# Kernel optimization log

Hardware: AMD Instinct MI355X
Metric: run time of the kernel (lower is better)

## Reference

```python
import jax, jax.numpy as jnp
import numpy as np

B, S, H, E, R, K = 8, 2048, 2048, 8, 16, 3
ALPHA = 0.5
LAMBDA_COV = 0.5
BETA_ENT = 0.1
TEMP_LO, TEMP_HI = 0.5, 1.5
SCALE_T = 2.0   # lora scaling (alpha/r) teacher
SCALE_S = 2.0   # lora scaling student
EPS = 1e-8


def setup_inputs() -> dict:
    key = jax.random.key(0)
    ks = jax.random.split(key, 16)
    tg = jax.random.uniform(ks[0], (B, S, E)) + 1e-3
    tg = tg / tg.sum(-1, keepdims=True)            # teacher gate probabilities
    sg = jax.random.uniform(ks[1], (B, S, E)) + 1e-3
    sg = sg / sg.sum(-1, keepdims=True)            # student gate probabilities
    th = jax.random.normal(ks[2], (B, S, H), jnp.float32)
    sh = jax.random.normal(ks[3], (B, S, H), jnp.float32)
    mask = jnp.ones((B, S), jnp.int32)
    un = jax.random.uniform(ks[4], (K, B, S, E))   # MC sampling noise
    inv = 1.0 / np.sqrt(H)
    W_t = jax.random.normal(ks[5], (H, H), jnp.float32) * inv
    b_t = jnp.zeros((H,), jnp.float32)
    A_t = jax.random.normal(ks[6], (R, H), jnp.float32) * 0.02
    B_t = jax.random.normal(ks[7], (E, H, R), jnp.float32) * 0.02
    W_s = jax.random.normal(ks[8], (H, H), jnp.float32) * inv
    b_s = jnp.zeros((H,), jnp.float32)
    A_s = jax.random.normal(ks[9], (R, H), jnp.float32) * 0.02
    B_s = jax.random.normal(ks[10], (E, H, R), jnp.float32) * 0.02
    temperature = jnp.float32(1.0)
    return dict(teacher_gates=tg, student_gates=sg,
                teacher_hidden_states=th, student_hidden_states=sh,
                attention_mask=mask, uniform_noise=un,
                W_t=W_t, b_t=b_t, A_t=A_t, B_t=B_t,
                W_s=W_s, b_s=b_s, A_s=A_s, B_s=B_s,
                temperature=temperature)


def _mse_all_experts(th, sh, W_t, b_t, A_t, B_t, W_s, b_s, A_s, B_s):
    """MSE(student_expert_hidden, teacher_expert_hidden) for ALL experts at once.
    expert_hidden = x@W^T + b + scale * (x@A^T) @ B_e^T. Expanding the squared
    difference avoids materializing [B,S,E,H]."""
    base_t = th @ W_t.T + b_t                      # [B,S,H]
    base_s = sh @ W_s.T + b_s                      # [B,S,H]
    a_t = th @ A_t.T                               # [B,S,R]
    a_s = sh @ A_s.T                               # [B,S,R]
    d = base_s - base_t                            # [B,S,H]
    mean_base = jnp.mean(d * d, axis=-1)           # [B,S]
    # cross terms: (1/H) d . (scale * a @ B_e^T)
    proj_s = jnp.einsum('bsh,ehr->bser', d, B_s)   # [B,S,E,R]
    proj_t = jnp.einsum('bsh,ehr->bser', d, B_t)
    cross = SCALE_S * jnp.einsum('bser,bsr->bse', proj_s, a_s) \
          - SCALE_T * jnp.einsum('bser,bsr->bse', proj_t, a_t)
    # quadratic lora terms via per-expert Gram matrices [E,R,R]
    G_ss = jnp.einsum('ehr,ehq->erq', B_s, B_s)
    G_st = jnp.einsum('ehr,ehq->erq', B_s, B_t)
    G_tt = jnp.einsum('ehr,ehq->erq', B_t, B_t)
    q_ss = jnp.einsum('bsr,erq,bsq->bse', a_s, G_ss, a_s)
    q_st = jnp.einsum('bsr,erq,bsq->bse', a_s, G_st, a_t)
    q_tt = jnp.einsum('bsr,erq,bsq->bse', a_t, G_tt, a_t)
    quad = SCALE_S * SCALE_S * q_ss - 2.0 * SCALE_S * SCALE_T * q_st + SCALE_T * SCALE_T * q_tt
    return mean_base[..., None] + (2.0 / H) * cross + (1.0 / H) * quad  # [B,S,E]


def _method_a(teacher_gates, student_gates, mse_all, uniform_noise, mask_f):
    """Vectorized MC expert sampling with alpha-renormalization (lax.scan over K)."""
    gumbel = -jnp.log(-jnp.log(uniform_noise * (1.0 - 2e-7) + 1e-7))  # [K,B,S,E]

    def step(p, g):  # p: current (renormalized) probs [B,S,E]
        idx = jnp.argmax(jnp.log(p) + g, axis=-1)          # multinomial sample [B,S]
        oh = jax.nn.one_hot(idx, E, dtype=p.dtype)          # [B,S,E]
        w = jnp.sum(p * oh, -1)                             # importance weight [B,S]
        mse_k = jnp.sum(mse_all * oh, -1)                   # gathered expert MSE
        sg_k = jnp.sum(student_gates * oh, -1)              # student gate at sampled expert
        mw = mask_f * w
        feat = jnp.sum(mw * mse_k)
        wsum = jnp.sum(mw)
        t_counts = jnp.sum(mw[..., None] * oh, axis=(0, 1))           # [E]
        s_counts = jnp.sum((mask_f * sg_k)[..., None] * oh, axis=(0, 1))
        p_new = p * (1.0 + (ALPHA - 1.0) * oh)
        p_new = p_new / jnp.sum(p_new, -1, keepdims=True)
        return p_new, (feat, wsum, t_counts, s_counts)

    _, (feats, wsums, tcs, scs) = jax.lax.scan(step, teacher_gates, gumbel)
    total_feat = feats.sum()
    total_w = wsums.sum()
    t_counts = tcs.sum(0)
    s_counts = scs.sum(0)

    feat_loss = total_feat / jnp.maximum(total_w, 1e-8)
    t_avg = t_counts / t_counts.sum() + EPS
    s_avg = s_counts / s_counts.sum() + EPS
    t_avg = t_avg / t_avg.sum()
    s_avg = s_avg / s_avg.sum()
    # F.kl_div(s.log(), t, reduction='batchmean') on 1-D input divides by E
    coverage_kl = jnp.sum(t_avg * (jnp.log(t_avg) - jnp.log(s_avg))) / E
    return feat_loss, coverage_kl


def reference(teacher_gates, student_gates, teacher_hidden_states, student_hidden_states,
              attention_mask, uniform_noise, W_t, b_t, A_t, B_t, W_s, b_s, A_s, B_s,
              temperature):
    mask_f = attention_mask.astype(teacher_gates.dtype)
    mse_all = _mse_all_experts(teacher_hidden_states, student_hidden_states,
                               W_t, b_t, A_t, B_t, W_s, b_s, A_s, B_s)
    feat_loss, coverage_kl = _method_a(teacher_gates, student_gates, mse_all,
                                       uniform_noise, mask_f)
    method_a_total = feat_loss + LAMBDA_COV * coverage_kl
    # Method B: temperature-entropy router distillation
    temp_c = jnp.clip(temperature, TEMP_LO, TEMP_HI)
    s_temp = jax.nn.softmax(student_gates / temp_c, axis=-1)
    # F.kl_div(s_temp.log(), teacher, 'batchmean') divides by batch dim B
    temp_kl = jnp.sum(teacher_gates * (jnp.log(teacher_gates) - jnp.log(s_temp))) / B
    entropy = -jnp.sum(student_gates * jnp.log(student_gates), axis=-1)
    entropy_loss = -jnp.mean(entropy)
    method_b_total = temp_kl + BETA_ENT * entropy_loss
    # [feat, coverage_kl, method_a_total, temp_kl, entropy, method_b_total, temperature]
    return jnp.stack([feat_loss, coverage_kl, method_a_total,
                      temp_kl, entropy_loss, method_b_total, temp_c])
```

## Files before the change

kernel.cpp:

```cpp
#include <hip/hip_runtime.h>
#include <math.h>

typedef unsigned short u16;
typedef unsigned int u32;
typedef float f32x4 __attribute__((ext_vector_type(4)));
typedef __bf16 bf16x8 __attribute__((ext_vector_type(8)));

#define NTOK 16384
#define HD   2048
#define KX   4096
#define NW   2176
#define NB   256

__device__ __forceinline__ u16 f2bf(float f) {
  u32 u = __float_as_uint(f);
  u32 r = (u + 0x7fffu + ((u >> 16) & 1u)) >> 16;
  return (u16)r;
}
__device__ __forceinline__ float bf2f(u16 s) { return __uint_as_float(((u32)s) << 16); }

__device__ __forceinline__ void gload_lds16(const void* g, void* l) {
  __builtin_amdgcn_global_load_lds((const __attribute__((address_space(1))) u32*)g,
                                   (__attribute__((address_space(3))) u32*)l, 16, 0, 0);
}

__global__ void zero_accum_k(float* a) {
  if (threadIdx.x < 32) a[threadIdx.x] = 0.f;
}

__global__ void make_bias_k(const float* __restrict__ b_t, const float* __restrict__ b_s,
                            float* __restrict__ db) {
  int i = blockIdx.x * 256 + threadIdx.x;
  if (i < HD) db[i] = b_s[i] - b_t[i];
}

__global__ __launch_bounds__(256) void convert_X_k(const float* __restrict__ th,
                                                   const float* __restrict__ sh,
                                                   u16* __restrict__ X) {
  size_t t = (size_t)blockIdx.x * 256 + threadIdx.x;
  int n = (int)(t >> 9);
  int k = ((int)t & 511) * 8;
  const float* src = (k < HD) ? (th + (size_t)n * HD + k) : (sh + (size_t)n * HD + (k - HD));
  float4 v0 = *(const float4*)src;
  float4 v1 = *(const float4*)(src + 4);
  uint4 pk;
  pk.x = (u32)f2bf(v0.x) | ((u32)f2bf(v0.y) << 16);
  pk.y = (u32)f2bf(v0.z) | ((u32)f2bf(v0.w) << 16);
  pk.z = (u32)f2bf(v1.x) | ((u32)f2bf(v1.y) << 16);
  pk.w = (u32)f2bf(v1.z) | ((u32)f2bf(v1.w) << 16);
  *(uint4*)(X + t * 8) = pk;
}

__global__ __launch_bounds__(256) void convert_W_k(const float* __restrict__ W_t,
                                                   const float* __restrict__ W_s,
                                                   const float* __restrict__ A_t,
                                                   const float* __restrict__ A_s,
                                                   u16* __restrict__ Wc) {
  size_t t = (size_t)blockIdx.x * 256 + threadIdx.x;
  int nr = (int)(t >> 9);
  int k = ((int)t & 511) * 8;
  float f[8];
#pragma unroll
  for (int j = 0; j < 8; ++j) f[j] = 0.f;
  if (nr < HD) {
    if (k < HD) {
      const float* s = W_t + (size_t)nr * HD + k;
#pragma unroll
      for (int j = 0; j < 8; ++j) f[j] = -s[j];
    } else {
      const float* s = W_s + (size_t)nr * HD + (k - HD);
#pragma unroll
      for (int j = 0; j < 8; ++j) f[j] = s[j];
    }
  } else if (nr < HD + 16) {
    if (k < HD) {
      const float* s = A_t + (size_t)(nr - HD) * HD + k;
#pragma unroll
      for (int j = 0; j < 8; ++j) f[j] = s[j];
    }
  } else if (nr < HD + 32) {
    if (k >= HD) {
      const float* s = A_s + (size_t)(nr - HD - 16) * HD + (k - HD);
#pragma unroll
      for (int j = 0; j < 8; ++j) f[j] = s[j];
    }
  }
  uint4 pk;
  pk.x = (u32)f2bf(f[0]) | ((u32)f2bf(f[1]) << 16);
  pk.y = (u32)f2bf(f[2]) | ((u32)f2bf(f[3]) << 16);
  pk.z = (u32)f2bf(f[4]) | ((u32)f2bf(f[5]) << 16);
  pk.w = (u32)f2bf(f[6]) | ((u32)f2bf(f[7]) << 16);
  *(uint4*)(Wc + t * 8) = pk;
}

__global__ __launch_bounds__(256) void convert_Bc_k(const float* __restrict__ Bs_,
                                                    const float* __restrict__ Bt_,
                                                    u16* __restrict__ Bc) {
  size_t t = (size_t)blockIdx.x * 256 + threadIdx.x;
  int c = (int)(t >> 8);
  int h = ((int)t & 255) * 8;
  const float* src = (c < 128) ? Bs_ : Bt_;
  int e = (c & 127) >> 4, r = c & 15;
  const float* base = src + (size_t)e * HD * 16 + (size_t)h * 16 + r;
  float f[8];
#pragma unroll
  for (int j = 0; j < 8; ++j) f[j] = base[(size_t)j * 16];
  uint4 pk;
  pk.x = (u32)f2bf(f[0]) | ((u32)f2bf(f[1]) << 16);
  pk.y = (u32)f2bf(f[2]) | ((u32)f2bf(f[3]) << 16);
  pk.z = (u32)f2bf(f[4]) | ((u32)f2bf(f[5]) << 16);
  pk.w = (u32)f2bf(f[6]) | ((u32)f2bf(f[7]) << 16);
  *(uint4*)(Bc + t * 8) = pk;
}

__global__ __launch_bounds__(256) void gram_k(const float* __restrict__ Bs_,
                                              const float* __restrict__ Bt_,
                                              float* __restrict__ grams) {
  __shared__ float ss[128 * 16];
  __shared__ float st[128 * 16];
  const int e = blockIdx.x;
  const int tid = threadIdx.x;
  const float* bs = Bs_ + (size_t)e * HD * 16;
  const float* bt = Bt_ + (size_t)e * HD * 16;
  const int r = tid >> 4, q = tid & 15;
  float gss = 0.f, gst = 0.f, gtt = 0.f;
  for (int h0 = 0; h0 < HD; h0 += 128) {
    __syncthreads();
#pragma unroll
    for (int j = 0; j < 8; ++j) {
      int i = tid + j * 256;
      ss[i] = bs[(size_t)h0 * 16 + i];
      st[i] = bt[(size_t)h0 * 16 + i];
    }
    __syncthreads();
    for (int hh = 0; hh < 128; ++hh) {
      float vsr = ss[hh * 16 + r], vsq = ss[hh * 16 + q];
      float vtr = st[hh * 16 + r], vtq = st[hh * 16 + q];
      gss += vsr * vsq;
      gst += vsr * vtq;
      gtt += vtr * vtq;
    }
  }
  grams[e * 256 + r * 16 + q] = gss;
  grams[2048 + e * 256 + r * 16 + q] = gst;
  grams[4096 + e * 256 + r * 16 + q] = gtt;
}

template <bool OUT_BF16>
__global__ __launch_bounds__(256) void gemm_bt_k(const u16* __restrict__ A, int lda,
                                                 const u16* __restrict__ Bm, int ldb,
                                                 int K, void* __restrict__ Cp, int ldc,
                                                 const float* __restrict__ bias, int bias_n) {
  __shared__ u16 As[128 * 32];
  __shared__ u16 Bs[128 * 32];
  const int tid = threadIdx.x;
  const int wave = tid >> 6;
  const int lane = tid & 63;
  const int m0 = blockIdx.x * 128;
  const int n0 = blockIdx.y * 128;
  const int wm = (wave >> 1) * 64;
  const int wn = (wave & 1) * 64;
  f32x4 acc[4][4] = {};

  const int srow = wave * 32 + (lane >> 2);
  const int scol = (lane & 3) * 8;
  const u16* gA = A + (size_t)(m0 + srow) * lda + scol;
  const u16* gB = Bm + (size_t)(n0 + srow) * ldb + scol;
  u16* lA = As + wave * 1024;
  u16* lB = Bs + wave * 1024;

  for (int k0 = 0; k0 < K; k0 += 32) {
    gload_lds16(gA + k0, lA);
    gload_lds16(gA + k0 + (size_t)16 * lda, lA + 512);
    gload_lds16(gB + k0, lB);
    gload_lds16(gB + k0 + (size_t)16 * ldb, lB + 512);
    __syncthreads();
    bf16x8 af[4], bff[4];
#pragma unroll
    for (int mi = 0; mi < 4; ++mi)
      af[mi] = *(const bf16x8*)&As[(wm + mi * 16 + (lane & 15)) * 32 + (lane >> 4) * 8];
#pragma unroll
    for (int ni = 0; ni < 4; ++ni)
      bff[ni] = *(const bf16x8*)&Bs[(wn + ni * 16 + (lane & 15)) * 32 + (lane >> 4) * 8];
#pragma unroll
    for (int mi = 0; mi < 4; ++mi)
#pragma unroll
      for (int ni = 0; ni < 4; ++ni)
        acc[mi][ni] = __builtin_amdgcn_mfma_f32_16x16x32_bf16(af[mi], bff[ni], acc[mi][ni], 0, 0, 0);
    __syncthreads();
  }

#pragma unroll
  for (int mi = 0; mi < 4; ++mi) {
#pragma unroll
    for (int ni = 0; ni < 4; ++ni) {
      int row0 = m0 + wm + mi * 16 + (lane >> 4) * 4;
      int col = n0 + wn + ni * 16 + (lane & 15);
      float badd = 0.f;
      if (bias != nullptr && col < bias_n) badd = bias[col];
      f32x4 v = acc[mi][ni];
#pragma unroll
      for (int j = 0; j < 4; ++j) {
        float x = v[j] + badd;
        if (OUT_BF16)
          ((u16*)Cp)[(size_t)(row0 + j) * ldc + col] = f2bf(x);
        else
          ((float*)Cp)[(size_t)(row0 + j) * ldc + col] = x;
      }
    }
  }
}

__global__ __launch_bounds__(256) void token_k(const u16* __restrict__ D,
                                               const float* __restrict__ proj,
                                               const float* __restrict__ grams,
                                               const float* __restrict__ tg,
                                               const float* __restrict__ sg,
                                               const float* __restrict__ un,
                                               const int* __restrict__ maskp,
                                               const float* __restrict__ temp,
                                               float* __restrict__ accum) {
  __shared__ float blk[20];
  if (threadIdx.x < 20) blk[threadIdx.x] = 0.f;
  __syncthreads();
  const int wave = threadIdx.x >> 6, lane = threadIdx.x & 63;
  const int n = blockIdx.x * 4 + wave;
  const u16* drow = D + (size_t)n * NW;

  float ssum = 0.f;
#pragma unroll
  for (int j = 0; j < 4; ++j) {
    uint4 v = *(const uint4*)(drow + j * 512 + lane * 8);
    u32 w;
    float f;
    w = v.x; f = bf2f((u16)(w & 0xffff)); ssum += f * f; f = bf2f((u16)(w >> 16)); ssum += f * f;
    w = v.y; f = bf2f((u16)(w & 0xffff)); ssum += f * f; f = bf2f((u16)(w >> 16)); ssum += f * f;
    w = v.z; f = bf2f((u16)(w & 0xffff)); ssum += f * f; f = bf2f((u16)(w >> 16)); ssum += f * f;
    w = v.w; f = bf2f((u16)(w & 0xffff)); ssum += f * f; f = bf2f((u16)(w >> 16)); ssum += f * f;
  }
#pragma unroll
  for (int m = 1; m < 64; m <<= 1) ssum += __shfl_xor(ssum, m);
  const float mean_base = ssum * (1.0f / (float)HD);

  float a_tv[16], a_sv[16];
#pragma unroll
  for (int r = 0; r < 16; ++r) {
    a_tv[r] = bf2f(drow[HD + r]);
    a_sv[r] = bf2f(drow[HD + 16 + r]);
  }

  const int e = lane & 7;
  const int pp = lane >> 3;
  const float* Ps = proj + (size_t)n * 256 + e * 16;
  const float* Pt = Ps + 128;
  const float* Gss = grams + e * 256;
  const float* Gst = grams + 2048 + e * 256;
  const float* Gtt = grams + 4096 + e * 256;
  float crossp = 0.f, qss = 0.f, qst = 0.f, qtt = 0.f;
#pragma unroll
  for (int rr = 0; rr < 2; ++rr) {
    int r = pp * 2 + rr;
    float asr = bf2f(drow[HD + 16 + r]);
    float atr = bf2f(drow[HD + r]);
    crossp += 2.0f * Ps[r] * asr - 2.0f * Pt[r] * atr;
    const float* gssr = Gss + r * 16;
    const float* gstr = Gst + r * 16;
    const float* gttr = Gtt + r * 16;
    float vss = 0.f, vst = 0.f, vtt = 0.f;
#pragma unroll
    for (int q = 0; q < 16; ++q) {
      vss += gssr[q] * a_sv[q];
      vst += gstr[q] * a_tv[q];
      vtt += gttr[q] * a_tv[q];
    }
    qss += asr * vss;
    qst += asr * vst;
    qtt += atr * vtt;
  }
#pragma unroll
  for (int m = 8; m < 64; m <<= 1) {
    crossp += __shfl_xor(crossp, m);
    qss += __shfl_xor(qss, m);
    qst += __shfl_xor(qst, m);
    qtt += __shfl_xor(qtt, m);
  }
  float quad = 4.0f * qss - 8.0f * qst + 4.0f * qtt;
  float my_mse = mean_base + (2.0f / (float)HD) * crossp + (1.0f / (float)HD) * quad;

  float p[8], gt[8], gs[8];
#pragma unroll
  for (int i = 0; i < 8; ++i) {
    gt[i] = tg[(size_t)n * 8 + i];
    gs[i] = sg[(size_t)n * 8 + i];
    p[i] = gt[i];
  }
  const float mf = (float)maskp[n];
  float feat = 0.f, wsum = 0.f;
  float tc[8] = {0, 0, 0, 0, 0, 0, 0, 0};
  float sc[8] = {0, 0, 0, 0, 0, 0, 0, 0};
#pragma unroll
  for (int k = 0; k < 3; ++k) {
    int idx = 0;
    float best = -1e30f;
#pragma unroll
    for (int i = 0; i < 8; ++i) {
      float u = un[((size_t)k * NTOK + n) * 8 + i];
      float g = -logf(-logf(u * (1.0f - 2e-7f) + 1e-7f));
      float s = logf(p[i]) + g;
      if (s > best) { best = s; idx = i; }
    }
    float w = 0.f, sgi = 0.f;
#pragma unroll
    for (int i = 0; i < 8; ++i)
      if (i == idx) { w = p[i]; sgi = gs[i]; }
    float mse_k = __shfl(my_mse, idx);
    feat += mf * w * mse_k;
    wsum += mf * w;
#pragma unroll
    for (int i = 0; i < 8; ++i)
      if (i == idx) { tc[i] += mf * w; sc[i] += mf * sgi; }
    float sum = 0.f;
#pragma unroll
    for (int i = 0; i < 8; ++i) {
      if (i == idx) p[i] *= 0.5f;
      sum += p[i];
    }
#pragma unroll
    for (int i = 0; i < 8; ++i) p[i] /= sum;
  }

  float tcl = fminf(fmaxf(temp[0], 0.5f), 1.5f);
  float invt = 1.0f / tcl;
  float x[8];
  float xm = -1e30f;
#pragma unroll
  for (int i = 0; i < 8; ++i) { x[i] = gs[i] * invt; xm = fmaxf(xm, x[i]); }
  float sx = 0.f;
#pragma unroll
  for (int i = 0; i < 8; ++i) sx += expf(x[i] - xm);
  float lse = xm + logf(sx);
  float tkl = 0.f, ent = 0.f;
#pragma unroll
  for (int i = 0; i < 8; ++i) {
    tkl += gt[i] * (logf(gt[i]) - (x[i] - lse));
    ent -= gs[i] * logf(gs[i]);
  }

  if (lane == 0) {
    atomicAdd(&blk[0], feat);
    atomicAdd(&blk[1], wsum);
#pragma unroll
    for (int i = 0; i < 8; ++i) {
      atomicAdd(&blk[2 + i], tc[i]);
      atomicAdd(&blk[10 + i], sc[i]);
    }
    atomicAdd(&blk[18], tkl);
    atomicAdd(&blk[19], ent);
  }
  __syncthreads();
  if (threadIdx.x < 20) atomicAdd(&accum[threadIdx.x], blk[threadIdx.x]);
}

__global__ void finalize_k(const float* __restrict__ accum, const float* __restrict__ temp,
                           float* __restrict__ out) {
  if (threadIdx.x != 0 || blockIdx.x != 0) return;
  float feat = accum[0] / fmaxf(accum[1], 1e-8f);
  float tsum = 0.f, ssum = 0.f;
  for (int e2 = 0; e2 < 8; ++e2) { tsum += accum[2 + e2]; ssum += accum[10 + e2]; }
  float ta[8], sa[8];
  float tas = 0.f, sas = 0.f;
  for (int e2 = 0; e2 < 8; ++e2) {
    ta[e2] = accum[2 + e2] / tsum + 1e-8f; tas += ta[e2];
    sa[e2] = accum[10 + e2] / ssum + 1e-8f; sas += sa[e2];
  }
  float cov = 0.f;
  for (int e2 = 0; e2 < 8; ++e2) {
    float tt = ta[e2] / tas, sv = sa[e2] / sas;
    cov += tt * (logf(tt) - logf(sv));
  }
  cov /= 8.0f;
  float tcl = fminf(fmaxf(temp[0], 0.5f), 1.5f);
  float tkl = accum[18] / 8.0f;
  float entl = -accum[19] / (float)NTOK;
  out[0] = feat;
  out[1] = cov;
  out[2] = feat + 0.5f * cov;
  out[3] = tkl;
  out[4] = entl;
  out[5] = tkl + 0.1f * entl;
  out[6] = tcl;
}

extern "C" void kernel_launch(void* const* d_in, const int* in_sizes, int n_in,
                              void* d_out, int out_size, void* d_ws, size_t ws_size,
                              hipStream_t stream) {
  const float* tg = (const float*)d_in[0];
  const float* sg = (const float*)d_in[1];
  const float* th = (const float*)d_in[2];
  const float* sh = (const float*)d_in[3];
  const int* mask = (const int*)d_in[4];
  const float* un = (const float*)d_in[5];
  const float* W_t = (const float*)d_in[6];
  const float* b_t = (const float*)d_in[7];
  const float* A_t = (const float*)d_in[8];
  const float* B_t = (const float*)d_in[9];
  const float* W_s = (const float*)d_in[10];
  const float* b_s = (const float*)d_in[11];
  const float* A_s = (const float*)d_in[12];
  const float* B_s = (const float*)d_in[13];
  const float* temp = (const float*)d_in[14];
  float* out = (float*)d_out;

  char* ws = (char*)d_ws;
  const size_t OFF_X = 0;
  const size_t OFF_W = OFF_X + (size_t)NTOK * KX * 2;
  const size_t OFF_D = OFF_W + (size_t)NW * KX * 2;
  const size_t OFF_BC = OFF_D + (size_t)NTOK * NW * 2;
  const size_t OFF_PJ = OFF_BC + (size_t)NB * HD * 2;
  const size_t OFF_GR = OFF_PJ + (size_t)NTOK * 256 * 4;
  const size_t OFF_AC = OFF_GR + 6144 * 4;
  const size_t OFF_BI = OFF_AC + 128;

  u16* X = (u16*)(ws + OFF_X);
  u16* Wc = (u16*)(ws + OFF_W);
  u16* D = (u16*)(ws + OFF_D);
  u16* Bc = (u16*)(ws + OFF_BC);
  float* proj = (float*)(ws + OFF_PJ);
  float* grams = (float*)(ws + OFF_GR);
  float* accum = (float*)(ws + OFF_AC);
  float* dbias = (float*)(ws + OFF_BI);

  zero_accum_k<<<1, 64, 0, stream>>>(accum);
  make_bias_k<<<8, 256, 0, stream>>>(b_t, b_s, dbias);
  convert_X_k<<<32768, 256, 0, stream>>>(th, sh, X);
  convert_W_k<<<4352, 256, 0, stream>>>(W_t, W_s, A_t, A_s, Wc);
  convert_Bc_k<<<256, 256, 0, stream>>>(B_s, B_t, Bc);
  gram_k<<<8, 256, 0, stream>>>(B_s, B_t, grams);

  gemm_bt_k<true><<<dim3(128, 17), 256, 0, stream>>>(X, KX, Wc, KX, KX, (void*)D, NW, dbias, HD);
  gemm_bt_k<false><<<dim3(128, 2), 256, 0, stream>>>(D, NW, Bc, HD, HD, (void*)proj, 256, nullptr, 0);

  token_k<<<4096, 256, 0, stream>>>(D, proj, grams, tg, sg, un, mask, temp, accum);
  finalize_k<<<1, 64, 0, stream>>>(accum, temp, out);
}
```

Before: 915.0 us.

## Add 256x256 double-buffered swizzled GEMM and split LoRA-A projection out

The main 16384x2176x4096 GEMM is replaced by a dedicated 256x256-tile kernel with 512 threads, double-buffered LDS via direct global-to-LDS loads, XOR swizzle against bank conflicts, grouped tile ordering and MFMA priority hints. The 32 LoRA-A columns are moved into their own small GEMM writing fp32, so the big GEMM works on an exact 2048-wide output with no padded 17th column tile. The gram kernel is split across 128 blocks that combine results with atomics. The larger tiles raise data reuse but use 64 KB of LDS and many registers per block, and the fp32 A projection slightly changes precision.

Measured after the change: 864.9 us. -5.5%, faster.

```diff
diff --git a/kernel.cpp b/kernel.cpp
--- a/kernel.cpp
+++ b/kernel.cpp
@@ -9,8 +9,6 @@
 #define NTOK 16384
 #define HD   2048
 #define KX   4096
-#define NW   2176
-#define NB   256
 
 __device__ __forceinline__ u16 f2bf(float f) {
   u32 u = __float_as_uint(f);
@@ -24,8 +22,9 @@
                                    (__attribute__((address_space(3))) u32*)l, 16, 0, 0);
 }
 
-__global__ void zero_accum_k(float* a) {
-  if (threadIdx.x < 32) a[threadIdx.x] = 0.f;
+__global__ void zero_k(float* a, int n) {
+  int i = blockIdx.x * 256 + threadIdx.x;
+  if (i < n) a[i] = 0.f;
 }
 
 __global__ void make_bias_k(const float* __restrict__ b_t, const float* __restrict__ b_s,
@@ -55,14 +54,17 @@
                                                    const float* __restrict__ W_s,
                                                    const float* __restrict__ A_t,
                                                    const float* __restrict__ A_s,
-                                                   u16* __restrict__ Wc) {
+                                                   u16* __restrict__ Wc,
+                                                   u16* __restrict__ WcA) {
   size_t t = (size_t)blockIdx.x * 256 + threadIdx.x;
   int nr = (int)(t >> 9);
   int k = ((int)t & 511) * 8;
   float f[8];
 #pragma unroll
   for (int j = 0; j < 8; ++j) f[j] = 0.f;
+  u16* dst;
   if (nr < HD) {
+    dst = Wc + (size_t)nr * KX + k;
     if (k < HD) {
       const float* s = W_t + (size_t)nr * HD + k;
 #pragma unroll
@@ -72,17 +74,21 @@
 #pragma unroll
       for (int j = 0; j < 8; ++j) f[j] = s[j];
     }
-  } else if (nr < HD + 16) {
-    if (k < HD) {
-      const float* s = A_t + (size_t)(nr - HD) * HD + k;
-#pragma unroll
-      for (int j = 0; j < 8; ++j) f[j] = s[j];
-    }
-  } else if (nr < HD + 32) {
-    if (k >= HD) {
-      const float* s = A_s + (size_t)(nr - HD - 16) * HD + (k - HD);
-#pragma unroll
-      for (int j = 0; j < 8; ++j) f[j] = s[j];
+  } else {
+    int nr2 = nr - HD;
+    dst = WcA + (size_t)nr2 * KX + k;
+    if (nr2 < 16) {
+      if (k < HD) {
+        const float* s = A_t + (size_t)nr2 * HD + k;
+#pragma unroll
+        for (int j = 0; j < 8; ++j) f[j] = s[j];
+      }
+    } else if (nr2 < 32) {
+      if (k >= HD) {
+        const float* s = A_s + (size_t)(nr2 - 16) * HD + (k - HD);
+#pragma unroll
+        for (int j = 0; j < 8; ++j) f[j] = s[j];
+      }
     }
   }
   uint4 pk;
@@ -90,7 +96,7 @@
   pk.y = (u32)f2bf(f[2]) | ((u32)f2bf(f[3]) << 16);
   pk.z = (u32)f2bf(f[4]) | ((u32)f2bf(f[5]) << 16);
   pk.w = (u32)f2bf(f[6]) | ((u32)f2bf(f[7]) << 16);
-  *(uint4*)(Wc + t * 8) = pk;
+  *(uint4*)dst = pk;
 }
 
 __global__ __launch_bounds__(256) void convert_Bc_k(const float* __restrict__ Bs_,
@@ -118,41 +124,132 @@
                                               float* __restrict__ grams) {
   __shared__ float ss[128 * 16];
   __shared__ float st[128 * 16];
-  const int e = blockIdx.x;
+  const int e = blockIdx.x >> 4;
+  const int ch = blockIdx.x & 15;
   const int tid = threadIdx.x;
-  const float* bs = Bs_ + (size_t)e * HD * 16;
-  const float* bt = Bt_ + (size_t)e * HD * 16;
+  const float* bs = Bs_ + (size_t)e * HD * 16 + (size_t)ch * 128 * 16;
+  const float* bt = Bt_ + (size_t)e * HD * 16 + (size_t)ch * 128 * 16;
+#pragma unroll
+  for (int j = 0; j < 8; ++j) {
+    int i = tid + j * 256;
+    ss[i] = bs[i];
+    st[i] = bt[i];
+  }
+  __syncthreads();
   const int r = tid >> 4, q = tid & 15;
   float gss = 0.f, gst = 0.f, gtt = 0.f;
-  for (int h0 = 0; h0 < HD; h0 += 128) {
+  for (int hh = 0; hh < 128; ++hh) {
+    float vsr = ss[hh * 16 + r], vsq = ss[hh * 16 + q];
+    float vtr = st[hh * 16 + r], vtq = st[hh * 16 + q];
+    gss += vsr * vsq;
+    gst += vsr * vtq;
+    gtt += vtr * vtq;
+  }
+  atomicAdd(&grams[e * 256 + r * 16 + q], gss);
+  atomicAdd(&grams[2048 + e * 256 + r * 16 + q], gst);
+  atomicAdd(&grams[4096 + e * 256 + r * 16 + q], gtt);
+}
+
+__global__ __launch_bounds__(512, 2) void gemm256_k(const u16* __restrict__ A,
+                                                    const u16* __restrict__ Bm,
+                                                    u16* __restrict__ D,
+                                                    const float* __restrict__ bias) {
+  __shared__ u16 As[2][16384];
+  __shared__ u16 Bs[2][16384];
+  const int tid = threadIdx.x;
+  const int w = tid >> 6, l = tid & 63;
+  const int id = blockIdx.x;
+  const int tile = (id & 7) * 64 + (id >> 3);
+  const int m0 = (tile & 63) * 256;
+  const int n0 = (tile >> 6) * 256;
+  const int wm = (w >> 2) * 128;
+  const int wn = (w & 3) * 64;
+
+  f32x4 acc[8][4] = {};
+
+  const int rlo = w * 8 + (l >> 3);
+  const int csw = ((l & 7) ^ (l >> 3)) * 8;
+  const u16* gA = A + (size_t)(m0 + rlo) * KX + csw;
+  const u16* gB = Bm + (size_t)(n0 + rlo) * KX + csw;
+
+  for (int t = 0; t < 64; ++t) {
+    const int b = t & 1;
+    if (t == 0) {
+#pragma unroll
+      for (int i = 0; i < 4; ++i) {
+        gload_lds16(gA + (size_t)i * 64 * KX, &As[0][i * 4096 + w * 512]);
+        gload_lds16(gB + (size_t)i * 64 * KX, &Bs[0][i * 4096 + w * 512]);
+      }
+    }
     __syncthreads();
-#pragma unroll
-    for (int j = 0; j < 8; ++j) {
-      int i = tid + j * 256;
-      ss[i] = bs[(size_t)h0 * 16 + i];
-      st[i] = bt[(size_t)h0 * 16 + i];
-    }
-    __syncthreads();
-    for (int hh = 0; hh < 128; ++hh) {
-      float vsr = ss[hh * 16 + r], vsq = ss[hh * 16 + q];
-      float vtr = st[hh * 16 + r], vtq = st[hh * 16 + q];
-      gss += vsr * vsq;
-      gst += vsr * vtq;
-      gtt += vtr * vtq;
-    }
-  }
-  grams[e * 256 + r * 16 + q] = gss;
-  grams[2048 + e * 256 + r * 16 + q] = gst;
-  grams[4096 + e * 256 + r * 16 + q] = gtt;
-}
-
-template <bool OUT_BF16>
+    if (t < 63) {
+      const u16* ga = gA + (size_t)(t + 1) * 64;
+      const u16* gb = gB + (size_t)(t + 1) * 64;
+#pragma unroll
+      for (int i = 0; i < 4; ++i) {
+        gload_lds16(ga + (size_t)i * 64 * KX, &As[b ^ 1][i * 4096 + w * 512]);
+        gload_lds16(gb + (size_t)i * 64 * KX, &Bs[b ^ 1][i * 4096 + w * 512]);
+      }
+    }
+#pragma unroll
+    for (int ks = 0; ks < 2; ++ks) {
+      bf16x8 bfr[4], afr[4];
+#pragma unroll
+      for (int n = 0; n < 4; ++n) {
+        int row = wn + n * 16 + (l & 15);
+        int off = (row * 64 + ks * 32 + (l >> 4) * 8) ^ ((row & 7) * 8);
+        bfr[n] = *(const bf16x8*)&Bs[b][off];
+      }
+#pragma unroll
+      for (int mm = 0; mm < 4; ++mm) {
+        int row = wm + mm * 16 + (l & 15);
+        int off = (row * 64 + ks * 32 + (l >> 4) * 8) ^ ((row & 7) * 8);
+        afr[mm] = *(const bf16x8*)&As[b][off];
+      }
+      __builtin_amdgcn_s_setprio(1);
+#pragma unroll
+      for (int mm = 0; mm < 4; ++mm)
+#pragma unroll
+        for (int n = 0; n < 4; ++n)
+          acc[mm][n] = __builtin_amdgcn_mfma_f32_16x16x32_bf16(afr[mm], bfr[n], acc[mm][n], 0, 0, 0);
+      __builtin_amdgcn_s_setprio(0);
+#pragma unroll
+      for (int mm = 0; mm < 4; ++mm) {
+        int row = wm + 64 + mm * 16 + (l & 15);
+        int off = (row * 64 + ks * 32 + (l >> 4) * 8) ^ ((row & 7) * 8);
+        afr[mm] = *(const bf16x8*)&As[b][off];
+      }
+      __builtin_amdgcn_s_setprio(1);
+#pragma unroll
+      for (int mm = 0; mm < 4; ++mm)
+#pragma unroll
+        for (int n = 0; n < 4; ++n)
+          acc[4 + mm][n] = __builtin_amdgcn_mfma_f32_16x16x32_bf16(afr[mm], bfr[n], acc[4 + mm][n], 0, 0, 0);
+      __builtin_amdgcn_s_setprio(0);
+    }
+  }
+
+#pragma unroll
+  for (int mi = 0; mi < 8; ++mi) {
+#pragma unroll
+    for (int ni = 0; ni < 4; ++ni) {
+      int row0 = m0 + wm + mi * 16 + (l >> 4) * 4;
+      int col = n0 + wn + ni * 16 + (l & 15);
+      float badd = bias[col];
+      f32x4 v = acc[mi][ni];
+#pragma unroll
+      for (int j = 0; j < 4; ++j)
+        D[(size_t)(row0 + j) * HD + col] = f2bf(v[j] + badd);
+    }
+  }
+}
+
 __global__ __launch_bounds__(256) void gemm_bt_k(const u16* __restrict__ A, int lda,
                                                  const u16* __restrict__ Bm, int ldb,
-                                                 int K, void* __restrict__ Cp, int ldc,
-                                                 const float* __restrict__ bias, int bias_n) {
-  __shared__ u16 As[128 * 32];
-  __shared__ u16 Bs[128 * 32];
+                                                 int K, float* __restrict__ Cp, int ldc,
+                                                 int store_n) {
+  __shared__ u16 Asl[128 * 32];
+  __shared__ u16 Bsl[128 * 32];
   const int tid = threadIdx.x;
   const int wave = tid >> 6;
   const int lane = tid & 63;
@@ -166,8 +263,8 @@
   const int scol = (lane & 3) * 8;
   const u16* gA = A + (size_t)(m0 + srow) * lda + scol;
   const u16* gB = Bm + (size_t)(n0 + srow) * ldb + scol;
-  u16* lA = As + wave * 1024;
-  u16* lB = Bs + wave * 1024;
+  u16* lA = Asl + wave * 1024;
+  u16* lB = Bsl + wave * 1024;
 
   for (int k0 = 0; k0 < K; k0 += 32) {
     gload_lds16(gA + k0, lA);
@@ -178,10 +275,10 @@
     bf16x8 af[4], bff[4];
 #pragma unroll
     for (int mi = 0; mi < 4; ++mi)
-      af[mi] = *(const bf16x8*)&As[(wm + mi * 16 + (lane & 15)) * 32 + (lane >> 4) * 8];
+      af[mi] = *(const bf16x8*)&Asl[(wm + mi * 16 + (lane & 15)) * 32 + (lane >> 4) * 8];
 #pragma unroll
     for (int ni = 0; ni < 4; ++ni)
-      bff[ni] = *(const bf16x8*)&Bs[(wn + ni * 16 + (lane & 15)) * 32 + (lane >> 4) * 8];
+      bff[ni] = *(const bf16x8*)&Bsl[(wn + ni * 16 + (lane & 15)) * 32 + (lane >> 4) * 8];
 #pragma unroll
     for (int mi = 0; mi < 4; ++mi)
 #pragma unroll
@@ -196,22 +293,18 @@
     for (int ni = 0; ni < 4; ++ni) {
       int row0 = m0 + wm + mi * 16 + (lane >> 4) * 4;
       int col = n0 + wn + ni * 16 + (lane & 15);
-      float badd = 0.f;
-      if (bias != nullptr && col < bias_n) badd = bias[col];
-      f32x4 v = acc[mi][ni];
-#pragma unroll
-      for (int j = 0; j < 4; ++j) {
-        float x = v[j] + badd;
-        if (OUT_BF16)
-          ((u16*)Cp)[(size_t)(row0 + j) * ldc + col] = f2bf(x);
-        else
-          ((float*)Cp)[(size_t)(row0 + j) * ldc + col] = x;
+      if (col < store_n) {
+        f32x4 v = acc[mi][ni];
+#pragma unroll
+        for (int j = 0; j < 4; ++j)
+          Cp[(size_t)(row0 + j) * ldc + col] = v[j];
       }
     }
   }
 }
 
 __global__ __launch_bounds__(256) void token_k(const u16* __restrict__ D,
+                                               const float* __restrict__ aV,
                                                const float* __restrict__ proj,
                                                const float* __restrict__ grams,
                                                const float* __restrict__ tg,
@@ -225,28 +318,29 @@
   __syncthreads();
   const int wave = threadIdx.x >> 6, lane = threadIdx.x & 63;
   const int n = blockIdx.x * 4 + wave;
-  const u16* drow = D + (size_t)n * NW;
+  const u16* drow = D + (size_t)n * HD;
 
   float ssum = 0.f;
 #pragma unroll
   for (int j = 0; j < 4; ++j) {
     uint4 v = *(const uint4*)(drow + j * 512 + lane * 8);
-    u32 w;
+    u32 wv;
     float f;
-    w = v.x; f = bf2f((u16)(w & 0xffff)); ssum += f * f; f = bf2f((u16)(w >> 16)); ssum += f * f;
-    w = v.y; f = bf2f((u16)(w & 0xffff)); ssum += f * f; f = bf2f((u16)(w >> 16)); ssum += f * f;
-    w = v.z; f = bf2f((u16)(w & 0xffff)); ssum += f * f; f = bf2f((u16)(w >> 16)); ssum += f * f;
-    w = v.w; f = bf2f((u16)(w & 0xffff)); ssum += f * f; f = bf2f((u16)(w >> 16)); ssum += f * f;
+    wv = v.x; f = bf2f((u16)(wv & 0xffff)); ssum += f * f; f = bf2f((u16)(wv >> 16)); ssum += f * f;
+    wv = v.y; f = bf2f((u16)(wv & 0xffff)); ssum += f * f; f = bf2f((u16)(wv >> 16)); ssum += f * f;
+    wv = v.z; f = bf2f((u16)(wv & 0xffff)); ssum += f * f; f = bf2f((u16)(wv >> 16)); ssum += f * f;
+    wv = v.w; f = bf2f((u16)(wv & 0xffff)); ssum += f * f; f = bf2f((u16)(wv >> 16)); ssum += f * f;
   }
 #pragma unroll
   for (int m = 1; m < 64; m <<= 1) ssum += __shfl_xor(ssum, m);
   const float mean_base = ssum * (1.0f / (float)HD);
 
+  const float* arow = aV + (size_t)n * 32;
   float a_tv[16], a_sv[16];
 #pragma unroll
   for (int r = 0; r < 16; ++r) {
-    a_tv[r] = bf2f(drow[HD + r]);
-    a_sv[r] = bf2f(drow[HD + 16 + r]);
+    a_tv[r] = arow[r];
+    a_sv[r] = arow[16 + r];
   }
 
   const int e = lane & 7;
@@ -260,8 +354,8 @@
 #pragma unroll
   for (int rr = 0; rr < 2; ++rr) {
     int r = pp * 2 + rr;
-    float asr = bf2f(drow[HD + 16 + r]);
-    float atr = bf2f(drow[HD + r]);
+    float asr = arow[16 + r];
+    float atr = arow[r];
     crossp += 2.0f * Ps[r] * asr - 2.0f * Pt[r] * atr;
     const float* gssr = Gss + r * 16;
     const float* gstr = Gst + r * 16;
@@ -309,16 +403,16 @@
       float s = logf(p[i]) + g;
       if (s > best) { best = s; idx = i; }
     }
-    float w = 0.f, sgi = 0.f;
+    float wgt = 0.f, sgi = 0.f;
 #pragma unroll
     for (int i = 0; i < 8; ++i)
-      if (i == idx) { w = p[i]; sgi = gs[i]; }
+      if (i == idx) { wgt = p[i]; sgi = gs[i]; }
     float mse_k = __shfl(my_mse, idx);
-    feat += mf * w * mse_k;
-    wsum += mf * w;
+    feat += mf * wgt * mse_k;
+    wsum += mf * wgt;
 #pragma unroll
     for (int i = 0; i < 8; ++i)
-      if (i == idx) { tc[i] += mf * w; sc[i] += mf * sgi; }
+      if (i == idx) { tc[i] += mf * wgt; sc[i] += mf * sgi; }
     float sum = 0.f;
 #pragma unroll
     for (int i = 0; i < 8; ++i) {
@@ -414,32 +508,37 @@
   char* ws = (char*)d_ws;
   const size_t OFF_X = 0;
   const size_t OFF_W = OFF_X + (size_t)NTOK * KX * 2;
-  const size_t OFF_D = OFF_W + (size_t)NW * KX * 2;
-  const size_t OFF_BC = OFF_D + (size_t)NTOK * NW * 2;
-  const size_t OFF_PJ = OFF_BC + (size_t)NB * HD * 2;
-  const size_t OFF_GR = OFF_PJ + (size_t)NTOK * 256 * 4;
+  const size_t OFF_WA = OFF_W + (size_t)HD * KX * 2;
+  const size_t OFF_D = OFF_WA + (size_t)128 * KX * 2;
+  const size_t OFF_BC = OFF_D + (size_t)NTOK * HD * 2;
+  const size_t OFF_PJ = OFF_BC + (size_t)256 * HD * 2;
+  const size_t OFF_AV = OFF_PJ + (size_t)NTOK * 256 * 4;
+  const size_t OFF_GR = OFF_AV + (size_t)NTOK * 32 * 4;
   const size_t OFF_AC = OFF_GR + 6144 * 4;
   const size_t OFF_BI = OFF_AC + 128;
 
   u16* X = (u16*)(ws + OFF_X);
   u16* Wc = (u16*)(ws + OFF_W);
+  u16* WcA = (u16*)(ws + OFF_WA);
   u16* D = (u16*)(ws + OFF_D);
   u16* Bc = (u16*)(ws + OFF_BC);
   float* proj = (float*)(ws + OFF_PJ);
+  float* aV = (float*)(ws + OFF_AV);
   float* grams = (float*)(ws + OFF_GR);
   float* accum = (float*)(ws + OFF_AC);
   float* dbias = (float*)(ws + OFF_BI);
 
-  zero_accum_k<<<1, 64, 0, stream>>>(accum);
+  zero_k<<<25, 256, 0, stream>>>(grams, 6176);
   make_bias_k<<<8, 256, 0, stream>>>(b_t, b_s, dbias);
   convert_X_k<<<32768, 256, 0, stream>>>(th, sh, X);
-  convert_W_k<<<4352, 256, 0, stream>>>(W_t, W_s, A_t, A_s, Wc);
+  convert_W_k<<<4352, 256, 0, stream>>>(W_t, W_s, A_t, A_s, Wc, WcA);
   convert_Bc_k<<<256, 256, 0, stream>>>(B_s, B_t, Bc);
-  gram_k<<<8, 256, 0, stream>>>(B_s, B_t, grams);
-
-  gemm_bt_k<true><<<dim3(128, 17), 256, 0, stream>>>(X, KX, Wc, KX, KX, (void*)D, NW, dbias, HD);
-  gemm_bt_k<false><<<dim3(128, 2), 256, 0, stream>>>(D, NW, Bc, HD, HD, (void*)proj, 256, nullptr, 0);
-
-  token_k<<<4096, 256, 0, stream>>>(D, proj, grams, tg, sg, un, mask, temp, accum);
+  gram_k<<<128, 256, 0, stream>>>(B_s, B_t, grams);
+
+  gemm256_k<<<512, 512, 0, stream>>>(X, Wc, D, dbias);
+  gemm_bt_k<<<dim3(128, 1), 256, 0, stream>>>(X, KX, WcA, KX, KX, aV, 32, 32);
+  gemm_bt_k<<<dim3(128, 2), 256, 0, stream>>>(D, HD, Bc, HD, HD, proj, 256, 256);
+
+  token_k<<<4096, 256, 0, stream>>>(D, aV, proj, grams, tg, sg, un, mask, temp, accum);
   finalize_k<<<1, 64, 0, stream>>>(accum, temp, out);
 }
```
